# Performance work log

Measured on AMD Instinct MI355X. Metric: run time of the kernel, lower is better.

## Reference

```python
import jax, jax.numpy as jnp
import numpy as np

B, D, H, W = 2, 32, 192, 192
N_SIGMA = 3
K = 8  # max instance id; ids are 1..K, 0 = background
FG_W = 1.0
W_INST, W_VAR, W_SEED = 1.0, 10.0, 1.0


def _make_xyzm():
    # channel 0 = x (varies along W), 1 = y (along H), 2 = z (along D); pixel_{x,y,z}=1
    xm = jnp.broadcast_to(jnp.linspace(0.0, 1.0, W).reshape(1, 1, W), (D, H, W))
    ym = jnp.broadcast_to(jnp.linspace(0.0, 1.0, H).reshape(1, H, 1), (D, H, W))
    zm = jnp.broadcast_to(jnp.linspace(0.0, 1.0, D).reshape(D, 1, 1), (D, H, W))
    return jnp.stack([xm, ym, zm], 0)  # (3, D, H, W)


def setup_inputs() -> dict:
    key = jax.random.key(0)
    k1, k2, k3, k4 = jax.random.split(key, 4)
    prediction = jax.random.normal(k1, (B, 3 + N_SIGMA + 1, D, H, W), jnp.float32)
    instances = jax.random.randint(k2, (B, D, H, W), 0, K + 1, jnp.int32)
    labels = jax.random.randint(k3, (B, D, H, W), 0, 2, jnp.int32)
    center_images = jax.random.uniform(k4, (B, D, H, W)) < 5e-4  # sparse center flags
    return {"prediction": prediction, "xyzm": _make_xyzm(),
            "instances": instances, "labels": labels, "center_images": center_images}


def _lovasz_hinge_flat(logits, labels):
    # logits, labels: (N,) flat; labels in {0,1} float
    signs = 2.0 * labels - 1.0
    errors = 1.0 - logits * signs
    order = jnp.argsort(-errors)          # descending errors
    errors_s = errors[order]
    gt_s = labels[order]
    gts = gt_s.sum()
    inter = gts - jnp.cumsum(gt_s)
    union = gts + jnp.cumsum(1.0 - gt_s)
    jacc = 1.0 - inter / union
    grad = jnp.concatenate([jacc[:1], jacc[1:] - jacc[:-1]])
    return jnp.dot(jax.nn.relu(errors_s), jax.lax.stop_gradient(grad))


def _forward(prediction, xyzm, instances, labels, center_images):
    def per_batch(pred, inst, lab, cim):
        emb = jnp.tanh(pred[0:3]) + xyzm                      # (3,D,H,W)
        sigma = pred[3:3 + N_SIGMA]                           # (ns,D,H,W)
        seed = jax.nn.sigmoid(pred[3 + N_SIGMA])              # (D,H,W)
        ids = jnp.arange(1, K + 1)
        masks = (inst[None] == ids[:, None, None, None]).astype(pred.dtype)  # (K,D,H,W)
        counts = masks.sum(axis=(1, 2, 3))                    # (K,)
        valid = counts > 0
        safe = jnp.maximum(counts, 1.0)
        # center: single flagged center voxel if exactly one, else masked mean of coords
        mean_center = jnp.einsum('kdhw,cdhw->kc', masks, xyzm) / safe[:, None]
        cmask = masks * cim[None].astype(pred.dtype)
        cm_cnt = cmask.sum(axis=(1, 2, 3))
        cm_center = jnp.einsum('kdhw,cdhw->kc', cmask, xyzm)
        center = jnp.where((cm_cnt == 1.0)[:, None], cm_center, mean_center)  # (K,3)
        # sigma stats per instance; var term vs detached mean, expanded form
        m_sig = jnp.einsum('kdhw,cdhw->kc', masks, sigma)
        m_sig2 = jnp.einsum('kdhw,cdhw->kc', masks, sigma * sigma)
        s_mean = m_sig / safe[:, None]                        # (K,ns)
        s_sg = jax.lax.stop_gradient(s_mean)
        var_sum = m_sig2 - 2.0 * s_sg * m_sig + s_sg * s_sg * counts[:, None]
        var_k = var_sum.sum(1) / (N_SIGMA * safe)
        s_exp = jnp.exp(10.0 * s_mean)                        # (K,ns)
        # sum_c s_c*(emb_c-center_c)^2, expanded to avoid a (K,3,D,H,W) temp
        d2 = (jnp.einsum('kc,cdhw->kdhw', s_exp, emb * emb)
              - 2.0 * jnp.einsum('kc,cdhw->kdhw', s_exp * center, emb)
              + (s_exp * center * center).sum(1)[:, None, None, None])
        dist = jnp.exp(-d2)                                   # (K,D,H,W)
        inst_k = jax.vmap(_lovasz_hinge_flat)(
            (2.0 * dist - 1.0).reshape(K, -1), masks.reshape(K, -1))
        obj = jnp.maximum(valid.sum(), 1).astype(pred.dtype)
        instance_loss = jnp.where(valid, inst_k, 0.0).sum() / obj
        var_loss = jnp.where(valid, var_k, 0.0).sum() / obj
        bg = (lab == 0).astype(pred.dtype)
        seed_loss = (bg * seed * seed).sum()
        seed_loss = seed_loss + FG_W * (masks * (seed[None] - jax.lax.stop_gradient(dist)) ** 2).sum()
        seed_loss = seed_loss / (D * H * W)
        return W_INST * instance_loss + W_VAR * var_loss + W_SEED * seed_loss

    losses = jax.vmap(per_batch)(prediction, instances, labels, center_images)
    return losses.mean()


def reference(prediction, xyzm, instances, labels, center_images):
    return _forward(prediction, xyzm, instances, labels, center_images)
```

## Files before the change

kernel.cpp:

```cpp
#include <hip/hip_runtime.h>
#include <stdint.h>

typedef unsigned long long u64;
typedef unsigned int u32;

#define BN 2
#define DD 32
#define HH 192
#define WW 192
#define NV (DD*HH*WW)
#define KK 8
#define NSL 288
#define VPB 4096
#define NB 256
#define BOFF 1808
#define L2E 1.44269504f
#define SSLOT 11
#define NFRONT 288

__device__ __forceinline__ u64 fx(float v){ return (u64)(long long)llrintf(v*4294967296.0f); }
__device__ __forceinline__ float unfx(u64 v){ return (float)((double)(long long)v*(1.0/4294967296.0)); }
__device__ __forceinline__ float rcp_f(float x){ return __builtin_amdgcn_rcpf(x); }
__device__ __forceinline__ float exp2_f(float x){ return __builtin_amdgcn_exp2f(x); }
__device__ __forceinline__ float tanh_f(float x){ return 1.f - 2.f*rcp_f(1.f + exp2_f(x*(2.f*L2E))); }
__device__ __forceinline__ float sigm_f(float x){ return rcp_f(1.f + exp2_f(-x*L2E)); }
__device__ __forceinline__ float rfl(float x){ return __uint_as_float(__builtin_amdgcn_readfirstlane((int)__float_as_uint(x))); }

struct Cell { float cnt, cmc, mx, my, mz, g0, g1, g2, h, cmx, cmy, cmz; };
__device__ __forceinline__ Cell load_cell(const u64* __restrict__ ssh, int bb, int kq){
    u64 st[SSLOT];
    #pragma unroll
    for (int s = 0; s < SSLOT; s++){
        u64 a = 0ull;
        #pragma unroll
        for (int sh = 0; sh < 4; sh++)
            a += ssh[((size_t)(sh*BN + bb)*KK + kq)*SSLOT + s];
        st[s] = a;
    }
    Cell c;
    c.cnt = (float)(long long)(st[0] >> 32);
    c.cmc = (float)(u32)st[0];
    c.mx = (float)(long long)st[1] * (1.f/(WW-1));
    c.my = (float)(long long)st[2] * (1.f/(HH-1));
    c.mz = (float)(long long)st[3] * (1.f/(DD-1));
    c.g0 = (float)((double)(long long)st[4] * (1.0/4096.0));
    c.g1 = (float)((double)(long long)st[5] * (1.0/4096.0));
    c.g2 = (float)((double)(long long)st[6] * (1.0/4096.0));
    c.h  = (float)((double)(long long)st[7] * (1.0/2048.0));
    c.cmx = unfx(st[8]); c.cmy = unfx(st[9]); c.cmz = unfx(st[10]);
    return c;
}

__global__ __launch_bounds__(512) void k_front(
        const u32* __restrict__ w, u32* __restrict__ fpart,
        u64* __restrict__ zero_base, int nzero_u64, u32* __restrict__ counter){
    int bid = blockIdx.x, t = threadIdx.x;
    if (bid == 0){
        for (int i = t; i < nzero_u64; i += 512) zero_base[i] = 0ull;
        if (t == 0) *counter = 0u;
    }
    __shared__ u32 sfl;
    if (t == 0) sfl = 0u;
    __syncthreads();
    const int chunk = (BN*NV/4)/NFRONT;
    u32 f = 0;
    for (int i = bid*chunk + t; i < (bid+1)*chunk; i += 512){
        u32 x = w[i];
        if (x == 0x3F800000u) f |= 1u;
        else if (x > 1u) f |= 2u;
        else if (x == 1u){ f |= 8u; if (i & 1) f |= 4u; }
    }
    if (f) atomicOr(&sfl, f);
    __syncthreads();
    if (t == 0) fpart[bid] = sfl;
}

__device__ __forceinline__ int decode_mode(int t, int nthr, const u32* __restrict__ fpart,
                                           u32* __restrict__ sfl){
    if (t == 0) *sfl = 0u;
    __syncthreads();
    u32 fo = 0;
    for (int i = t; i < NFRONT; i += nthr) fo |= fpart[i];
    if (fo) atomicOr(sfl, fo);
    __syncthreads();
    u32 fl = *sfl;
    __syncthreads();
    return (fl & 1u) ? 2 : ((fl & 2u) ? 1 : ((fl & 4u) ? 0 : ((fl & 8u) ? 3 : 0)));
}

__global__ __launch_bounds__(1024, 8) void k_stats(
        const float* __restrict__ pred, const int* __restrict__ inst,
        const void* __restrict__ cim, const u32* __restrict__ fpart,
        u64* __restrict__ ssh){
    int sx = blockIdx.x, b = blockIdx.y;
    __shared__ u64 bins[16][4][25];
    __shared__ u64 cmb[16][KK][4];
    __shared__ u32 sfl;
    for (int i = threadIdx.x; i < 16*4*25; i += 1024) ((u64*)bins)[i] = 0ull;
    for (int i = threadIdx.x; i < 16*KK*4; i += 1024) ((u64*)cmb)[i] = 0ull;
    int mode = decode_mode(threadIdx.x, 1024, fpart, &sfl);
    const float* pb = pred + (size_t)b*7*NV;
    const int* ib = inst + (size_t)b*NV;
    int t = threadIdx.x;
    int wv = t >> 6, lp = t & 3;
    int g = sx*VPB + t*4;

    float4 s0v = *(const float4*)&pb[3*(size_t)NV + g];
    float4 s1v = *(const float4*)&pb[4*(size_t)NV + g];
    float4 s2v = *(const float4*)&pb[5*(size_t)NV + g];
    int4 iv4 = *(const int4*)&ib[g];
    int iy = g / WW;
    int ix = g - iy*WW;
    int iz = iy / HH; iy -= iz*HH;
    u64 fxm = fx(ix*(1.f/(WW-1)));
    u64 fdx = fx(1.f/(WW-1));
    u64 fym = fx(iy*(1.f/(HH-1)));
    u64 fzm = fx(iz*(1.f/(DD-1)));
    u32 cv4 = 0;
    size_t gi = (size_t)b*NV + g;
    if (mode == 0){
        int4 c = *(const int4*)&((const int*)cim)[gi];
        cv4 = (c.x?1u:0u)|(c.y?2u:0u)|(c.z?4u:0u)|(c.w?8u:0u);
    } else if (mode == 1){
        u32 c = *(const u32*)&((const unsigned char*)cim)[gi];
        cv4 = ((c&0xFFu)?1u:0u)|((c&0xFF00u)?2u:0u)|((c&0xFF0000u)?4u:0u)|((c&0xFF000000u)?8u:0u);
    } else if (mode == 2){
        float4 c = *(const float4*)&((const float*)cim)[gi];
        cv4 = (c.x!=0.f?1u:0u)|(c.y!=0.f?2u:0u)|(c.z!=0.f?4u:0u)|(c.w!=0.f?8u:0u);
    } else {
        int4 c0 = *(const int4*)&((const int*)cim)[2*gi];
        int4 c1 = *(const int4*)&((const int*)cim)[2*gi + 4];
        cv4 = (c0.x?1u:0u)|(c0.z?2u:0u)|(c1.x?4u:0u)|(c1.z?8u:0u);
    }
    float s0a[4] = {s0v.x,s0v.y,s0v.z,s0v.w};
    float s1a[4] = {s1v.x,s1v.y,s1v.z,s1v.w};
    float s2a[4] = {s2v.x,s2v.y,s2v.z,s2v.w};
    int iva[4] = {iv4.x,iv4.y,iv4.z,iv4.w};
    #pragma unroll
    for (int j = 0; j < 4; j++){
        int iv = iva[j];
        if (iv >= 1 && iv <= KK){
            u64* bn = &bins[wv][lp][(iv-1)*3];
            u32 cv = (cv4 >> j) & 1u;
            u32 q0 = (u32)llrintf((s0a[j] + 16.f)*4096.f);
            u32 q1 = (u32)llrintf((s1a[j] + 16.f)*4096.f);
            u32 q2 = (u32)llrintf((s2a[j] + 16.f)*4096.f);
            float s2t = s0a[j]*s0a[j] + s1a[j]*s1a[j] + s2a[j]*s2a[j];
            u32 r = (u32)llrintf(fminf(s2t, 512.f)*2048.f);
            atomicAdd(&bn[0], (1ull << 44) | ((u64)(u32)(ix + j) << 24) | ((u64)(u32)iy << 4) | cv);
            atomicAdd(&bn[1], ((u64)q0 << 32) | q1);
            atomicAdd(&bn[2], ((u64)q2 << 32) | r);
            if (cv){
                u64* cb = &cmb[wv][iv-1][0];
                atomicAdd(&cb[0], fxm + (u64)j*fdx);
                atomicAdd(&cb[1], fym);
                atomicAdd(&cb[2], fzm);
            }
        }
    }
    __syncthreads();
    u64* cell0 = &ssh[((size_t)((sx&3)*BN + b))*KK*SSLOT];
    if (t < KK){
        int k = t;
        u64 sA = 0ull, sB = 0ull, sC = 0ull;
        #pragma unroll
        for (int r2 = 0; r2 < 64; r2++){
            const u64* bn = &bins[r2>>2][r2&3][k*3];
            sA += bn[0]; sB += bn[1]; sC += bn[2];
        }
        u64 cnt = sA >> 44;
        if (cnt){
            u64 six = (sA >> 24) & 0xFFFFFull;
            u64 siy = (sA >> 4) & 0xFFFFFull;
            u64 cm  = sA & 0xFull;
            long long bias = (long long)(cnt * 65536ull);
            long long g0 = (long long)(sB >> 32) - bias;
            long long g1 = (long long)(sB & 0xFFFFFFFFull) - bias;
            long long g2 = (long long)(sC >> 32) - bias;
            u64 h = sC & 0xFFFFFFFFull;
            u64* cell = cell0 + (size_t)k*SSLOT;
            atomicAdd(&cell[0], (cnt << 32) | cm);
            atomicAdd(&cell[1], six);
            atomicAdd(&cell[2], siy);
            atomicAdd(&cell[3], cnt*(u64)iz);
            atomicAdd(&cell[4], (u64)g0);
            atomicAdd(&cell[5], (u64)g1);
            atomicAdd(&cell[6], (u64)g2);
            atomicAdd(&cell[7], h);
        }
    }
    if (t < KK*3){
        int k = t / 3, s = t - k*3;
        u64 acc = 0ull;
        #pragma unroll
        for (int w = 0; w < 16; w++) acc += cmb[w][k][s];
        if (acc) atomicAdd(&cell0[(size_t)k*SSLOT + 8 + s], acc);
    }
}

__global__ __launch_bounds__(1024, 8) void k_hist(
        const u64* __restrict__ ssh, const float* __restrict__ pred,
        const int* __restrict__ inst, const int* __restrict__ lab,
        u32* __restrict__ hs, u64* __restrict__ bgsh){
    __shared__ u32 lh[KK*2*NB];
    __shared__ u64 fgfx, bgfx;
    __shared__ float dv[KK*6];
    int sx = blockIdx.x, b = blockIdx.y;
    int t = threadIdx.x;
    if (t == 0){ fgfx = 0ull; bgfx = 0ull; }
    for (int i = t; i < KK*2*NB; i += 1024) lh[i] = 0u;
    if (t < KK){
        int kq = t;
        Cell c = load_cell(ssh, b, kq);
        float safe = fmaxf(c.cnt, 1.f);
        float isafe = 1.f/safe;
        float c0 = (c.cmc == 1.f) ? c.cmx : c.mx*isafe;
        float c1 = (c.cmc == 1.f) ? c.cmy : c.my*isafe;
        float c2 = (c.cmc == 1.f) ? c.cmz : c.mz*isafe;
        dv[kq*6+0] = expf(10.f*c.g0*isafe)*L2E;
        dv[kq*6+1] = expf(10.f*c.g1*isafe)*L2E;
        dv[kq*6+2] = expf(10.f*c.g2*isafe)*L2E;
        dv[kq*6+3] = c0; dv[kq*6+4] = c1; dv[kq*6+5] = c2;
    }
    __syncthreads();
    float ax[KK], ay[KK], az[KK], cx[KK], cy[KK], cz[KK];
    #pragma unroll
    for (int k = 0; k < KK; k++){
        ax[k]=rfl(dv[k*6+0]); ay[k]=rfl(dv[k*6+1]); az[k]=rfl(dv[k*6+2]);
        cx[k]=rfl(dv[k*6+3]); cy[k]=rfl(dv[k*6+4]); cz[k]=rfl(dv[k*6+5]);
    }
    const float* pb = pred + (size_t)b*7*NV;
    const int* ib = inst + (size_t)b*NV;
    const int* lb = lab + (size_t)b*NV;
    int g = sx*VPB + t*4;
    float4 p0 = *(const float4*)&pb[g];
    float4 p1 = *(const float4*)&pb[(size_t)NV + g];
    float4 p2 = *(const float4*)&pb[2*(size_t)NV + g];
    float4 p6 = *(const float4*)&pb[6*(size_t)NV + g];
    int4 iv4 = *(const int4*)&ib[g];
    int4 lb4 = *(const int4*)&lb[g];
    int iy = g / WW;
    int ix = g - iy*WW;
    int iz = iy / HH; iy -= iz*HH;
    float xm = ix*(1.f/(WW-1)), ym = iy*(1.f/(HH-1)), zm = iz*(1.f/(DD-1));
    float p0a[4] = {p0.x,p0.y,p0.z,p0.w};
    float p1a[4] = {p1.x,p1.y,p1.z,p1.w};
    float p2a[4] = {p2.x,p2.y,p2.z,p2.w};
    float p6a[4] = {p6.x,p6.y,p6.z,p6.w};
    int iva[4] = {iv4.x,iv4.y,iv4.z,iv4.w};
    int lba[4] = {lb4.x,lb4.y,lb4.z,lb4.w};
    float e0[4], e1[4], e2[4], sd[4];
    float bgacc = 0.f;
    #pragma unroll
    for (int j = 0; j < 4; j++){
        e0[j] = tanh_f(p0a[j]) + xm + j*(1.f/(WW-1));
        e1[j] = tanh_f(p1a[j]) + ym;
        e2[j] = tanh_f(p2a[j]) + zm;
        sd[j] = sigm_f(p6a[j]);
        if (lba[j] == 0) bgacc += sd[j]*sd[j];
    }
    float fgacc = 0.f;
    #pragma unroll
    for (int k = 0; k < KK; k++){
        #pragma unroll
        for (int j = 0; j < 4; j++){
            float d0 = e0[j] - cx[k], d1 = e1[j] - cy[k], dz = e2[j] - cz[k];
            float d2 = ax[k]*d0*d0;
            d2 = fmaf(ay[k]*d1, d1, d2);
            d2 = fmaf(az[k]*dz, dz, d2);
            float dist = exp2_f(-d2);
            if (iva[j] == k + 1){
                float e = fmaf(-2.f, dist, 2.f);
                int bu = (int)(__float_as_uint(e) >> 19) - BOFF;
                bu = bu < 0 ? 0 : (bu > NB-1 ? NB-1 : bu);
                atomicAdd(&lh[k*512 + bu], 1u);
                fgacc += (sd[j] - dist)*(sd[j] - dist);
            } else {
                int bu = (int)(__float_as_uint(dist) >> 19) - (BOFF - 16);
                bu = bu < 0 ? 0 : (bu > NB-1 ? NB-1 : bu);
                atomicAdd(&lh[k*512 + NB + bu], 1u);
            }
        }
    }
    #pragma unroll
    for (int off = 32; off > 0; off >>= 1){
        fgacc += __shfl_down(fgacc, off);
        bgacc += __shfl_down(bgacc, off);
    }
    if ((t & 63) == 0){
        if (fgacc != 0.f) atomicAdd(&fgfx, fx(fgacc));
        if (bgacc != 0.f) atomicAdd(&bgfx, fx(bgacc));
    }
    __syncthreads();
    if (t == 0){
        if (bgfx) atomicAdd(&bgsh[(size_t)b*8 + (sx&7)], bgfx);
        if (fgfx) atomicAdd(&bgsh[(size_t)(2+b)*8 + (sx&7)], fgfx);
    }
    u32* out = hs + ((size_t)b*NSL + sx)*(KK*NB);
    for (int i = t; i < KK*NB; i += 1024){
        int k = i >> 8, bu = i & 255;
        out[i] = (lh[k*512 + bu] << 16) | lh[k*512 + NB + bu];
    }
}

__global__ __launch_bounds__(1024) void k_lovasz(
        const u32* __restrict__ hs, const u64* __restrict__ ssh,
        float* __restrict__ lov, const u64* __restrict__ bgsh,
        u32* __restrict__ counter, float* __restrict__ out){
    int bk = blockIdx.x, b = bk >> 3, k = bk & 7;
    int t = threadIdx.x;
    __shared__ float s_cnt[16], s_vrk[16], s_val[16];
    if (t < 16){
        Cell c = load_cell(ssh, t >> 3, t & 7);
        float safe = fmaxf(c.cnt, 1.f);
        float isafe = 1.f/safe;
        float sm0 = c.g0*isafe, sm1 = c.g1*isafe, sm2 = c.g2*isafe;
        float vs = c.h - 2.f*(sm0*c.g0 + sm1*c.g1 + sm2*c.g2)
                 + (sm0*sm0 + sm1*sm1 + sm2*sm2)*c.cnt;
        s_vrk[t] = vs*isafe*(1.f/3.f);
        s_val[t] = c.cnt > 0.f ? 1.f : 0.f;
        s_cnt[t] = c.cnt;
    }
    __syncthreads();
    float gts = s_cnt[bk];
    float obj = fmaxf(s_val[b*8+0]+s_val[b*8+1]+s_val[b*8+2]+s_val[b*8+3]
                     +s_val[b*8+4]+s_val[b*8+5]+s_val[b*8+6]+s_val[b*8+7], 1.f);
    float coef = s_val[bk]/obj;
    float lv = 0.f;
    __shared__ u64 part[4][NB];
    __shared__ u64 wsum[4];
    __shared__ float racc[NB];
    if (gts >= 0.5f){
        int bu = (NB - 1) - (t & 255);
        int sg = t >> 8;
        u32 np = 0, nn = 0;
        const u32* base = hs + (size_t)b*NSL*(KK*NB) + k*NB + bu;
        for (int s = sg; s < NSL; s += 4){
            u32 h = base[(size_t)s*(KK*NB)];
            np += h >> 16; nn += h & 0xFFFFu;
        }
        part[sg][t & 255] = ((u64)np << 32) | nn;
        __syncthreads();
        u64 pack = 0ull, inc = 0ull;
        if (t < NB){
            pack = part[0][t] + part[1][t] + part[2][t] + part[3][t];
            int lane = t & 63;
            inc = pack;
            #pragma unroll
            for (int off = 1; off < 64; off <<= 1){
                u64 n = __shfl_up(inc, off);
                if (lane >= off) inc += n;
            }
            if (lane == 63) wsum[t >> 6] = inc;
        }
        __syncthreads();
        if (t < 4){
            u64 x = wsum[t];
            #pragma unroll
            for (int off = 1; off < 4; off <<= 1){
                u64 n = __shfl_up(x, off);
                if (t >= off) x += n;
            }
            wsum[t] = x;
        }
        __syncthreads();
        float acc = 0.f;
        if (t < NB){
            int wid = t >> 6;
            u64 excl = inc - pack + (wid ? wsum[wid - 1] : 0ull);
            u32 np2 = (u32)(pack >> 32), nn2 = (u32)pack;
            if (np2 | nn2){
                int bu2 = (NB - 1) - t;
                float Pe = (float)(u32)(excl >> 32), Qe = (float)(u32)excl;
                float Pi = Pe + (float)np2, Qi = Qe + (float)nn2;
                float je = 1.f - (gts - Pe)/(gts + Qe);
                float ji = 1.f - (gts - Pi)/(gts + Qi);
                u32 bits = ((u32)(bu2 + BOFF) << 19) | (1u << 18);
                if (bits > 0x40000000u) bits = 0x40000000u;
                acc = __uint_as_float(bits) * (ji - je);
            }
            racc[t] = acc;
        }
        __syncthreads();
        for (int off = 128; off > 0; off >>= 1){
            if (t < off) racc[t] += racc[t + off];
            __syncthreads();
        }
        lv = coef * racc[0];
    }
    if (t == 0){
        __hip_atomic_store(&lov[bk], lv, __ATOMIC_RELEASE, __HIP_MEMORY_SCOPE_AGENT);
        u32 ticket = __hip_atomic_fetch_add(counter, 1u, __ATOMIC_ACQ_REL, __HIP_MEMORY_SCOPE_AGENT);
        if (ticket == 15u){
            float tot = 0.f;
            for (int i = 0; i < 16; i++)
                tot += __hip_atomic_load(&lov[i], __ATOMIC_ACQUIRE, __HIP_MEMORY_SCOPE_AGENT);
            for (int b2 = 0; b2 < BN; b2++){
                float objb = fmaxf(s_val[b2*8+0]+s_val[b2*8+1]+s_val[b2*8+2]+s_val[b2*8+3]
                                  +s_val[b2*8+4]+s_val[b2*8+5]+s_val[b2*8+6]+s_val[b2*8+7], 1.f);
                float vp = 0.f;
                for (int kq = 0; kq < 8; kq++) vp += s_val[b2*8+kq]*s_vrk[b2*8+kq];
                float bg = 0.f, fg = 0.f;
                for (int sh = 0; sh < 8; sh++){
                    bg += unfx(bgsh[(size_t)b2*8 + sh]);
                    fg += unfx(bgsh[(size_t)(2+b2)*8 + sh]);
                }
                tot += 10.f*vp/objb + (bg + fg)*(1.f/(float)NV);
            }
            out[0] = tot * 0.5f;
        }
    }
}

extern "C" void kernel_launch(void* const* d_in, const int* in_sizes, int n_in,
                              void* d_out, int out_size, void* d_ws, size_t ws_size,
                              hipStream_t stream){
    const float* pred = (const float*)d_in[0];
    const int*   inst = (const int*)d_in[2];
    const int*   lab  = (const int*)d_in[3];
    const void*  cim  = d_in[4];

    char* ws = (char*)d_ws;
    size_t off = 0;
    u32* hs = (u32*)(ws + off);        off += (size_t)BN*NSL*KK*NB*4;
    size_t zero0 = off;
    u64* ssh = (u64*)(ws + off);       off += (size_t)4*BN*KK*SSLOT*8;
    u64* bgsh = (u64*)(ws + off);      off += (size_t)4*8*8;
    int nzero_u64 = (int)((off - zero0)/8);
    float* lov = (float*)(ws + off);   off += 16*4;
    u32* counter = (u32*)(ws + off);   off += 4;
    u32* fpart = (u32*)(ws + off);     off += NFRONT*4;

    k_front<<<dim3(NFRONT), dim3(512), 0, stream>>>((const u32*)cim, fpart, ssh, nzero_u64, counter);
    k_stats<<<dim3(NSL, BN), dim3(1024), 0, stream>>>(pred, inst, cim, fpart, ssh);
    k_hist<<<dim3(NSL, BN), dim3(1024), 0, stream>>>(ssh, pred, inst, lab, hs, bgsh);
    k_lovasz<<<16, 1024, 0, stream>>>(hs, ssh, lov, bgsh, counter, (float*)d_out);
}
```

Baseline: 69.29 us.

## Merge slice histograms with sharded global atomics and add far-distance fast path

```diff
diff --git a/kernel.cpp b/kernel.cpp
--- a/kernel.cpp
+++ b/kernel.cpp
@@ -55,9 +55,11 @@
         const u32* __restrict__ w, u32* __restrict__ fpart,
         u64* __restrict__ zero_base, int nzero_u64, u32* __restrict__ counter){
     int bid = blockIdx.x, t = threadIdx.x;
-    if (bid == 0){
-        for (int i = t; i < nzero_u64; i += 512) zero_base[i] = 0ull;
-        if (t == 0) *counter = 0u;
+    if (bid < 16){
+        int nz16 = (nzero_u64 + 15) >> 4;
+        int lo = bid*nz16, hi = min(lo + nz16, nzero_u64);
+        for (int i = lo + t; i < hi; i += 512) zero_base[i] = 0ull;
+        if (bid == 0 && t == 0) *counter = 0u;
     }
     __shared__ u32 sfl;
     if (t == 0) sfl = 0u;
@@ -201,7 +203,7 @@
 __global__ __launch_bounds__(1024, 8) void k_hist(
         const u64* __restrict__ ssh, const float* __restrict__ pred,
         const int* __restrict__ inst, const int* __restrict__ lab,
-        u32* __restrict__ hs, u64* __restrict__ bgsh){
+        u32* __restrict__ ph, u64* __restrict__ bgsh){
     __shared__ u32 lh[KK*2*NB];
     __shared__ u64 fgfx, bgfx;
     __shared__ float dv[KK*6];
@@ -262,23 +264,35 @@
     float fgacc = 0.f;
     #pragma unroll
     for (int k = 0; k < KK; k++){
+        float d2L[4];
         #pragma unroll
         for (int j = 0; j < 4; j++){
             float d0 = e0[j] - cx[k], d1 = e1[j] - cy[k], dz = e2[j] - cz[k];
             float d2 = ax[k]*d0*d0;
             d2 = fmaf(ay[k]*d1, d1, d2);
             d2 = fmaf(az[k]*dz, dz, d2);
-            float dist = exp2_f(-d2);
-            if (iva[j] == k + 1){
-                float e = fmaf(-2.f, dist, 2.f);
-                int bu = (int)(__float_as_uint(e) >> 19) - BOFF;
-                bu = bu < 0 ? 0 : (bu > NB-1 ? NB-1 : bu);
-                atomicAdd(&lh[k*512 + bu], 1u);
-                fgacc += (sd[j] - dist)*(sd[j] - dist);
-            } else {
-                int bu = (int)(__float_as_uint(dist) >> 19) - (BOFF - 16);
-                bu = bu < 0 ? 0 : (bu > NB-1 ? NB-1 : bu);
-                atomicAdd(&lh[k*512 + NB + bu], 1u);
+            d2L[j] = d2;
+        }
+        bool anymask = (iva[0] == k+1) | (iva[1] == k+1) | (iva[2] == k+1) | (iva[3] == k+1);
+        float dmin = fminf(fminf(d2L[0], d2L[1]), fminf(d2L[2], d2L[3]));
+        bool fast = (dmin > 15.f) && !anymask;
+        if (__all(fast)){
+            if ((t & 63) == 0) atomicAdd(&lh[k*512 + NB], 256u);
+        } else {
+            #pragma unroll
+            for (int j = 0; j < 4; j++){
+                float dist = exp2_f(-d2L[j]);
+                if (iva[j] == k + 1){
+                    float e = fmaf(-2.f, dist, 2.f);
+                    int bu = (int)(__float_as_uint(e) >> 19) - BOFF;
+                    bu = bu < 0 ? 0 : (bu > NB-1 ? NB-1 : bu);
+                    atomicAdd(&lh[k*512 + bu], 1u);
+                    fgacc += (sd[j] - dist)*(sd[j] - dist);
+                } else {
+                    int bu = (int)(__float_as_uint(dist) >> 19) - (BOFF - 16);
+                    bu = bu < 0 ? 0 : (bu > NB-1 ? NB-1 : bu);
+                    atomicAdd(&lh[k*512 + NB + bu], 1u);
+                }
             }
         }
     }
@@ -296,18 +310,21 @@
         if (bgfx) atomicAdd(&bgsh[(size_t)b*8 + (sx&7)], bgfx);
         if (fgfx) atomicAdd(&bgsh[(size_t)(2+b)*8 + (sx&7)], fgfx);
     }
-    u32* out = hs + ((size_t)b*NSL + sx)*(KK*NB);
-    for (int i = t; i < KK*NB; i += 1024){
-        int k = i >> 8, bu = i & 255;
-        out[i] = (lh[k*512 + bu] << 16) | lh[k*512 + NB + bu];
-    }
-}
-
-__global__ __launch_bounds__(1024) void k_lovasz(
-        const u32* __restrict__ hs, const u64* __restrict__ ssh,
+    u32* phb = ph + ((size_t)(sx&3)*16 + (size_t)b*KK)*2*NB;
+    for (int i = t; i < KK*2*NB; i += 1024){
+        u32 v = lh[i];
+        if (v){
+            int k = i >> 9, rem = i & 511;
+            atomicAdd(&phb[(size_t)k*2*NB + rem], v);
+        }
+    }
+}
+
+__global__ __launch_bounds__(256) void k_lovasz(
+        const u32* __restrict__ ph, const u64* __restrict__ ssh,
         float* __restrict__ lov, const u64* __restrict__ bgsh,
         u32* __restrict__ counter, float* __restrict__ out){
-    int bk = blockIdx.x, b = bk >> 3, k = bk & 7;
+    int bk = blockIdx.x, b = bk >> 3;
     int t = threadIdx.x;
     __shared__ float s_cnt[16], s_vrk[16], s_val[16];
     if (t < 16){
@@ -327,32 +344,25 @@
                      +s_val[b*8+4]+s_val[b*8+5]+s_val[b*8+6]+s_val[b*8+7], 1.f);
     float coef = s_val[bk]/obj;
     float lv = 0.f;
-    __shared__ u64 part[4][NB];
     __shared__ u64 wsum[4];
     __shared__ float racc[NB];
     if (gts >= 0.5f){
-        int bu = (NB - 1) - (t & 255);
-        int sg = t >> 8;
+        int bu = (NB - 1) - t;
         u32 np = 0, nn = 0;
-        const u32* base = hs + (size_t)b*NSL*(KK*NB) + k*NB + bu;
-        for (int s = sg; s < NSL; s += 4){
-            u32 h = base[(size_t)s*(KK*NB)];
-            np += h >> 16; nn += h & 0xFFFFu;
-        }
-        part[sg][t & 255] = ((u64)np << 32) | nn;
-        __syncthreads();
-        u64 pack = 0ull, inc = 0ull;
-        if (t < NB){
-            pack = part[0][t] + part[1][t] + part[2][t] + part[3][t];
-            int lane = t & 63;
-            inc = pack;
-            #pragma unroll
-            for (int off = 1; off < 64; off <<= 1){
-                u64 n = __shfl_up(inc, off);
-                if (lane >= off) inc += n;
-            }
-            if (lane == 63) wsum[t >> 6] = inc;
-        }
+        #pragma unroll
+        for (int sh = 0; sh < 4; sh++){
+            const u32* base = ph + ((size_t)sh*16 + bk)*2*NB;
+            np += base[bu]; nn += base[NB + bu];
+        }
+        u64 pack = ((u64)np << 32) | nn;
+        int lane = t & 63, wid = t >> 6;
+        u64 inc = pack;
+        #pragma unroll
+        for (int off = 1; off < 64; off <<= 1){
+            u64 n = __shfl_up(inc, off);
+            if (lane >= off) inc += n;
+        }
+        if (lane == 63) wsum[wid] = inc;
         __syncthreads();
         if (t < 4){
             u64 x = wsum[t];
@@ -364,23 +374,18 @@
             wsum[t] = x;
         }
         __syncthreads();
+        u64 excl = inc - pack + (wid ? wsum[wid - 1] : 0ull);
         float acc = 0.f;
-        if (t < NB){
-            int wid = t >> 6;
-            u64 excl = inc - pack + (wid ? wsum[wid - 1] : 0ull);
-            u32 np2 = (u32)(pack >> 32), nn2 = (u32)pack;
-            if (np2 | nn2){
-                int bu2 = (NB - 1) - t;
-                float Pe = (float)(u32)(excl >> 32), Qe = (float)(u32)excl;
-                float Pi = Pe + (float)np2, Qi = Qe + (float)nn2;
-                float je = 1.f - (gts - Pe)/(gts + Qe);
-                float ji = 1.f - (gts - Pi)/(gts + Qi);
-                u32 bits = ((u32)(bu2 + BOFF) << 19) | (1u << 18);
-                if (bits > 0x40000000u) bits = 0x40000000u;
-                acc = __uint_as_float(bits) * (ji - je);
-            }
-            racc[t] = acc;
-        }
+        if (np | nn){
+            float Pe = (float)(u32)(excl >> 32), Qe = (float)(u32)excl;
+            float Pi = Pe + (float)np, Qi = Qe + (float)nn;
+            float je = 1.f - (gts - Pe)/(gts + Qe);
+            float ji = 1.f - (gts - Pi)/(gts + Qi);
+            u32 bits = ((u32)(bu + BOFF) << 19) | (1u << 18);
+            if (bits > 0x40000000u) bits = 0x40000000u;
+            acc = __uint_as_float(bits) * (ji - je);
+        }
+        racc[t] = acc;
         __syncthreads();
         for (int off = 128; off > 0; off >>= 1){
             if (t < off) racc[t] += racc[t + off];
@@ -422,10 +427,10 @@
 
     char* ws = (char*)d_ws;
     size_t off = 0;
-    u32* hs = (u32*)(ws + off);        off += (size_t)BN*NSL*KK*NB*4;
     size_t zero0 = off;
     u64* ssh = (u64*)(ws + off);       off += (size_t)4*BN*KK*SSLOT*8;
     u64* bgsh = (u64*)(ws + off);      off += (size_t)4*8*8;
+    u32* ph = (u32*)(ws + off);        off += (size_t)4*16*2*NB*4;
     int nzero_u64 = (int)((off - zero0)/8);
     float* lov = (float*)(ws + off);   off += 16*4;
     u32* counter = (u32*)(ws + off);   off += 4;
@@ -433,6 +438,6 @@
 
     k_front<<<dim3(NFRONT), dim3(512), 0, stream>>>((const u32*)cim, fpart, ssh, nzero_u64, counter);
     k_stats<<<dim3(NSL, BN), dim3(1024), 0, stream>>>(pred, inst, cim, fpart, ssh);
-    k_hist<<<dim3(NSL, BN), dim3(1024), 0, stream>>>(ssh, pred, inst, lab, hs, bgsh);
-    k_lovasz<<<16, 1024, 0, stream>>>(hs, ssh, lov, bgsh, counter, (float*)d_out);
-}
+    k_hist<<<dim3(NSL, BN), dim3(1024), 0, stream>>>(ssh, pred, inst, lab, ph, bgsh);
+    k_lovasz<<<16, 256, 0, stream>>>(ph, ssh, lov, bgsh, counter, (float*)d_out);
+}
```

Measured after the change: 67.57 us. 2.5% less time.
